# Optimization experiments

Hardware: AMD Instinct MI355X
Metric: run time of the kernel (lower is better)

The kernel has to match this reference:

```python
import jax, jax.numpy as jnp
import numpy as np

EPS = 1e-6
STRIDE = 2  # kv_pool_stride
NUM_HEADS = 8

def _layernorm(x, w, b):
    mu = jnp.mean(x, axis=-1, keepdims=True)
    var = jnp.mean(jnp.square(x - mu), axis=-1, keepdims=True)
    return (x - mu) * jax.lax.rsqrt(var + EPS) * w + b

def setup_inputs() -> dict:
    key = jax.random.key(0)
    B, H, W, C = 8, 56, 56, 384
    hidden = int(C * 2.0)
    ks = jax.random.split(key, 12)
    s = 0.02
    return {
        "x": jax.random.normal(ks[0], (B, H * W, C), jnp.float32),
        "ln1_w": jnp.ones((C,), jnp.float32),
        "ln1_b": jnp.zeros((C,), jnp.float32),
        "qw": jax.random.normal(ks[1], (C, C), jnp.float32) * s,
        "qb": jnp.zeros((C,), jnp.float32),
        "kw": jax.random.normal(ks[2], (C, C), jnp.float32) * s,
        "kb": jnp.zeros((C,), jnp.float32),
        "vw": jax.random.normal(ks[3], (C, C), jnp.float32) * s,
        "vb": jnp.zeros((C,), jnp.float32),
        "pw": jax.random.normal(ks[4], (C, C), jnp.float32) * s,
        "pb": jnp.zeros((C,), jnp.float32),
        "ln2_w": jnp.ones((C,), jnp.float32),
        "ln2_b": jnp.zeros((C,), jnp.float32),
        "fc1_w": jax.random.normal(ks[5], (C, hidden), jnp.float32) * s,
        "fc1_b": jnp.zeros((hidden,), jnp.float32),
        "fc2_w": jax.random.normal(ks[6], (hidden, C), jnp.float32) * s,
        "fc2_b": jnp.zeros((C,), jnp.float32),
        "H": 56,
        "W": 56,
    }

def reference(x, ln1_w, ln1_b, qw, qb, kw, kb, vw, vb, pw, pb,
              ln2_w, ln2_b, fc1_w, fc1_b, fc2_w, fc2_b, H, W):
    B, N, C = x.shape
    h = NUM_HEADS
    d = C // h
    scale = d ** -0.5

    # Attention branch: Q from norm1(x); K,V from RAW x (as in source), KV avg-pooled 2x2
    q_tok = _layernorm(x, ln1_w, ln1_b)
    s = STRIDE
    Hk, Wk = H // s, W // s
    kv = x.reshape(B, Hk, s, Wk, s, C).mean(axis=(2, 4)).reshape(B, Hk * Wk, C)

    q = (q_tok @ qw + qb).reshape(B, N, h, d)
    k = (kv @ kw + kb).reshape(B, Hk * Wk, h, d)
    v = (kv @ vw + vb).reshape(B, Hk * Wk, h, d)

    attn = jnp.einsum('bqhd,bkhd->bhqk', q, k) * scale
    attn = jax.nn.softmax(attn, axis=-1)
    out = jnp.einsum('bhqk,bkhd->bqhd', attn, v).reshape(B, N, C)
    x = x + (out @ pw + pb)

    # MLP branch (GELU exact, matching torch nn.GELU default)
    y = _layernorm(x, ln2_w, ln2_b)
    y = jax.nn.gelu(y @ fc1_w + fc1_b, approximate=False)
    x = x + (y @ fc2_w + fc2_b)
    return x
```

## Files before the change

kernel.cpp:

```cpp
#include <hip/hip_runtime.h>
#include <math.h>

#define B_    8
#define N_TOK 3136
#define C_    384
#define DH    48
#define NK    784
#define HID   768
#define M1    25088
#define M2    6272
#define M1Q   6272

typedef unsigned short u16;
typedef __attribute__((ext_vector_type(8))) short bf16x8;
typedef __attribute__((ext_vector_type(4))) float f32x4;

__device__ __forceinline__ float b2f(u16 u) {
  return __uint_as_float(((unsigned)u) << 16);
}
__device__ __forceinline__ u16 f2b(float f) {
  unsigned u = __float_as_uint(f);
  return (u16)((u + 0x7fffu + ((u >> 16) & 1u)) >> 16);
}
__device__ __forceinline__ u16 f2b_trunc(float f) {
  return (u16)(__float_as_uint(f) >> 16);
}
__device__ __forceinline__ void gload_lds16(const u16* g, u16* l) {
  __builtin_amdgcn_global_load_lds(
      (const __attribute__((address_space(1))) void*)g,
      (__attribute__((address_space(3))) void*)l, 16, 0, 0);
}

__global__ __launch_bounds__(256) void ln1_pool(
    const float* __restrict__ X, const float* __restrict__ w,
    const float* __restrict__ b, u16* __restrict__ Y, u16* __restrict__ KV) {
  if (blockIdx.x < M1 / 4) {
    const int row = blockIdx.x * 4 + (threadIdx.x >> 6);
    const int lane = threadIdx.x & 63;
    const size_t base = (size_t)row * C_;
    float v[6];
#pragma unroll
    for (int i = 0; i < 6; ++i) v[i] = X[base + lane + 64 * i];
    float s = 0.f;
#pragma unroll
    for (int i = 0; i < 6; ++i) s += v[i];
#pragma unroll
    for (int off = 32; off > 0; off >>= 1) s += __shfl_xor(s, off);
    const float mu = s * (1.0f / C_);
    float q = 0.f;
#pragma unroll
    for (int i = 0; i < 6; ++i) { float d = v[i] - mu; q += d * d; }
#pragma unroll
    for (int off = 32; off > 0; off >>= 1) q += __shfl_xor(q, off);
    const float r = rsqrtf(q * (1.0f / C_) + 1e-6f);
#pragma unroll
    for (int i = 0; i < 6; ++i) {
      int c = lane + 64 * i;
      Y[base + c] = f2b((v[i] - mu) * r * w[c] + b[c]);
    }
  } else {
    int t = (blockIdx.x - M1 / 4) * 256 + threadIdx.x;
    if (t >= M2 * C_) return;
    int c = t % C_;
    int row = t / C_;
    int bb = row / NK;
    int rr = row - bb * NK;
    int hk = rr / 28;
    int wk = rr - hk * 28;
    const float* p = X + ((size_t)(bb * N_TOK + hk * 112 + wk * 2)) * C_ + c;
    KV[t] = f2b(0.25f * (p[0] + p[C_] + p[56 * C_] + p[57 * C_]));
  }
}

__global__ __launch_bounds__(256) void ln2_rows(const u16* __restrict__ X,
    const float* __restrict__ w, const float* __restrict__ b, u16* __restrict__ Y) {
  const int row = blockIdx.x * 4 + (threadIdx.x >> 6);
  const int lane = threadIdx.x & 63;
  const size_t base = (size_t)row * C_;
  float v[6];
#pragma unroll
  for (int i = 0; i < 6; ++i) v[i] = b2f(X[base + lane + 64 * i]);
  float s = 0.f;
#pragma unroll
  for (int i = 0; i < 6; ++i) s += v[i];
#pragma unroll
  for (int off = 32; off > 0; off >>= 1) s += __shfl_xor(s, off);
  const float mu = s * (1.0f / C_);
  float q = 0.f;
#pragma unroll
  for (int i = 0; i < 6; ++i) { float d = v[i] - mu; q += d * d; }
#pragma unroll
  for (int off = 32; off > 0; off >>= 1) q += __shfl_xor(q, off);
  const float r = rsqrtf(q * (1.0f / C_) + 1e-6f);
#pragma unroll
  for (int i = 0; i < 6; ++i) {
    int c = lane + 64 * i;
    Y[base + c] = f2b((v[i] - mu) * r * w[c] + b[c]);
  }
}

struct TransArgs {
  const float* src[6];
  u16* dst[6];
  int K[6], N[6], tx[6], ty[6];
};
__global__ __launch_bounds__(256) void transpose_all(TransArgs a) {
  const int id = blockIdx.z;
  if ((int)blockIdx.x >= a.tx[id] || (int)blockIdx.y >= a.ty[id]) return;
  const float* W = a.src[id];
  u16* WT = a.dst[id];
  const int K = a.K[id], N = a.N[id];
  __shared__ u16 tile[64][73];
  const int k0 = blockIdx.y * 64, n0 = blockIdx.x * 64;
  for (int i = threadIdx.x; i < 64 * 64; i += 256) {
    int kk = i >> 6, nn = i & 63;
    tile[kk][nn] = f2b(W[(size_t)(k0 + kk) * N + n0 + nn]);
  }
  __syncthreads();
  for (int i = threadIdx.x; i < 64 * 64; i += 256) {
    int nn = i >> 6, kk = i & 63;
    WT[(size_t)(n0 + nn) * K + k0 + kk] = tile[kk][nn];
  }
}

template<int EPI, bool RES32, bool OUT32>
__device__ __forceinline__ void gemm_core(
    const u16* __restrict__ A, const u16* __restrict__ BT,
    const float* __restrict__ bias, const void* __restrict__ resv,
    void* __restrict__ Cv, int N, int K, int m0, int n0) {
  __shared__ u16 As[128 * 64];
  __shared__ u16 Bs[128 * 64];
  const int tid  = threadIdx.x;
  const int wave = tid >> 6;
  const int lane = tid & 63;
  const int quad = lane >> 4;
  const int ll   = lane & 15;
  const int wm   = wave >> 1, wn = wave & 1;

  const int srow = wave * 32 + (lane >> 3);
  const int sgs  = lane & 7;

  f32x4 acc[4][4];
#pragma unroll
  for (int i = 0; i < 4; ++i)
#pragma unroll
    for (int j = 0; j < 4; ++j) acc[i][j] = (f32x4){0.f, 0.f, 0.f, 0.f};

  for (int kk0 = 0; kk0 < K; kk0 += 64) {
    __syncthreads();
#pragma unroll
    for (int c = 0; c < 4; ++c) {
      const int r = srow + c * 8;
      const int g = sgs ^ (r & 7);
      gload_lds16(A  + (size_t)(m0 + r) * K + kk0 + g * 8,
                  As + (size_t)(wave * 32 + c * 8) * 64);
      gload_lds16(BT + (size_t)(n0 + r) * K + kk0 + g * 8,
                  Bs + (size_t)(wave * 32 + c * 8) * 64);
    }
    __syncthreads();
#pragma unroll
    for (int ks = 0; ks < 2; ++ks) {
      const int gsw = (quad + 4 * ks) ^ (ll & 7);
      bf16x8 af[4], bfr[4];
#pragma unroll
      for (int im = 0; im < 4; ++im)
        af[im] = *(const bf16x8*)&As[(size_t)(wm * 64 + im * 16 + ll) * 64 + gsw * 8];
#pragma unroll
      for (int jn = 0; jn < 4; ++jn)
        bfr[jn] = *(const bf16x8*)&Bs[(size_t)(wn * 64 + jn * 16 + ll) * 64 + gsw * 8];
#pragma unroll
      for (int im = 0; im < 4; ++im)
#pragma unroll
        for (int jn = 0; jn < 4; ++jn)
          acc[im][jn] = __builtin_amdgcn_mfma_f32_16x16x32_bf16(
              af[im], bfr[jn], acc[im][jn], 0, 0, 0);
    }
  }

  float bb[4];
#pragma unroll
  for (int jn = 0; jn < 4; ++jn) bb[jn] = bias[n0 + wn * 64 + jn * 16 + ll];
#pragma unroll
  for (int im = 0; im < 4; ++im) {
    const int row = m0 + wm * 64 + im * 16 + quad * 4;
#pragma unroll
    for (int jn = 0; jn < 4; ++jn) {
      const int col = n0 + wn * 64 + jn * 16 + ll;
#pragma unroll
      for (int r = 0; r < 4; ++r) {
        float o = acc[im][jn][r] + bb[jn];
        if (EPI == 1) {
          o = 0.5f * o * (1.0f + erff(o * 0.70710678118654752f));
        } else if (EPI == 2) {
          size_t ri = (size_t)(row + r) * N + col;
          o += RES32 ? ((const float*)resv)[ri] : b2f(((const u16*)resv)[ri]);
        }
        if (OUT32) ((float*)Cv)[(size_t)(row + r) * N + col] = o;
        else       ((u16*)Cv)[(size_t)(row + r) * N + col] = f2b(o);
      }
    }
  }
}

template<int EPI, bool RES32, bool OUT32>
__global__ __launch_bounds__(256) void gemm_bt(
    const u16* __restrict__ A, const u16* __restrict__ BT,
    const float* __restrict__ bias, const void* __restrict__ resv,
    void* __restrict__ Cv, int N, int K) {
  gemm_core<EPI, RES32, OUT32>(A, BT, bias, resv, Cv, N, K,
                               blockIdx.y << 7, blockIdx.x << 7);
}

struct QKVArgs {
  const u16* A[3];
  const u16* BT[3];
  const float* bias[3];
  u16* C[3];
  int M[3];
};
__global__ __launch_bounds__(256) void gemm_qkv(QKVArgs a) {
  const int z = blockIdx.z;
  const int m0 = blockIdx.y << 7;
  if (m0 >= a.M[z]) return;
  gemm_core<0, false, false>(a.A[z], a.BT[z], a.bias[z], nullptr, a.C[z],
                             C_, C_, m0, blockIdx.x << 7);
}

#define QS_STR 72
__global__ __launch_bounds__(512) void attn_mfma(
    const u16* __restrict__ Q, const u16* __restrict__ Kb,
    const u16* __restrict__ Vb, u16* __restrict__ O) {
  __shared__ u16 Ks[2][64 * 64];
  __shared__ u16 Vt[2][48 * QS_STR];
  __shared__ u16 Ps[128 * QS_STR];
  const int tid  = threadIdx.x;
  const int wave = tid >> 6;
  const int lane = tid & 63;
  const int quad = lane >> 4;
  const int ll   = lane & 15;
  const int qt   = blockIdx.x;
  const int bh   = blockIdx.y;
  const int b    = bh >> 3, h = bh & 7;
  const int q0   = qt * 128;
  const float scale = 0.14433756729740643f;

  bf16x8 af0, af1;
  {
    int qrow = q0 + wave * 16 + ll;
    if (qrow >= N_TOK) qrow = N_TOK - 1;
    const u16* qp = Q + ((size_t)(b * N_TOK) + qrow) * C_ + h * DH;
    af0 = *(const bf16x8*)(qp + quad * 8);
    if (quad < 2) af1 = *(const bf16x8*)(qp + 32 + quad * 8);
    else          af1 = (bf16x8){0, 0, 0, 0, 0, 0, 0, 0};
  }

  const int krow = (wave << 3) + (lane >> 3);
  const int kgrp = (lane & 7) ^ (lane >> 3);
  const size_t kbase_g = (size_t)(b * NK) * C_ + h * DH + kgrp * 8;

  uint4 vreg;

  {
    int kk = krow; if (kk >= NK) kk = NK - 1;
    gload_lds16(Kb + kbase_g + (size_t)kk * C_, &Ks[0][wave << 9]);
    if (wave < 6) {
      int vk = lane; if (vk >= NK) vk = NK - 1;
      vreg = *(const uint4*)(Vb + ((size_t)(b * NK) + vk) * C_ + h * DH + wave * 8);
      const u16* vp = (const u16*)&vreg;
#pragma unroll
      for (int j = 0; j < 8; ++j)
        Vt[0][(wave * 8 + j) * QS_STR + lane] = vp[j];
    }
  }
  __syncthreads();

  f32x4 Ofr[3] = {{0.f,0.f,0.f,0.f},{0.f,0.f,0.f,0.f},{0.f,0.f,0.f,0.f}};
  float lrow[4] = {0.f, 0.f, 0.f, 0.f};

  for (int t = 0; t < 13; ++t) {
    const int cur = t & 1, nxt = cur ^ 1;
    const int kbase = t * 64;

    if (t < 12) {
      const int knext = kbase + 64;
      int kk = knext + krow; if (kk >= NK) kk = NK - 1;
      gload_lds16(Kb + kbase_g + (size_t)kk * C_, &Ks[nxt][wave << 9]);
      if (wave < 6) {
        int vk = knext + lane; if (vk >= NK) vk = NK - 1;
        vreg = *(const uint4*)(Vb + ((size_t)(b * NK) + vk) * C_ + h * DH + wave * 8);
      }
    }

    f32x4 S[4];
#pragma unroll
    for (int nt = 0; nt < 4; ++nt) {
      const int rb = (nt * 16 + ll) * 64;
      bf16x8 b0 = *(const bf16x8*)&Ks[cur][rb + ((quad    ) ^ (ll & 7)) * 8];
      bf16x8 b1 = *(const bf16x8*)&Ks[cur][rb + ((quad + 4) ^ (ll & 7)) * 8];
      f32x4 acc = {0.f, 0.f, 0.f, 0.f};
      acc = __builtin_amdgcn_mfma_f32_16x16x32_bf16(af0, b0, acc, 0, 0, 0);
      acc = __builtin_amdgcn_mfma_f32_16x16x32_bf16(af1, b1, acc, 0, 0, 0);
      if (kbase + nt * 16 + ll >= NK)
        acc = (f32x4){-1e30f, -1e30f, -1e30f, -1e30f};
      S[nt] = acc;
    }

#pragma unroll
    for (int nt = 0; nt < 4; ++nt) {
      const int g = nt * 2 + (ll >> 3);
      const int gp = g ^ quad;
#pragma unroll
      for (int r = 0; r < 4; ++r) {
        float p = __expf(S[nt][r] * scale);
        lrow[r] += p;
        Ps[(wave * 16 + quad * 4 + r) * QS_STR + (gp << 3) + (ll & 7)] = f2b_trunc(p);
      }
    }

#pragma unroll
    for (int dt = 0; dt < 3; ++dt)
#pragma unroll
      for (int ks = 0; ks < 2; ++ks) {
        const int gp = ((ks << 2) + quad) ^ ((ll >> 2) & 3);
        bf16x8 a = *(const bf16x8*)&Ps[(wave * 16 + ll) * QS_STR + (gp << 3)];
        bf16x8 bb = *(const bf16x8*)&Vt[cur][(dt * 16 + ll) * QS_STR + ks * 32 + quad * 8];
        Ofr[dt] = __builtin_amdgcn_mfma_f32_16x16x32_bf16(a, bb, Ofr[dt], 0, 0, 0);
      }

    if (t < 12 && wave < 6) {
      const u16* vp = (const u16*)&vreg;
#pragma unroll
      for (int j = 0; j < 8; ++j)
        Vt[nxt][(wave * 8 + j) * QS_STR + lane] = vp[j];
    }
    __syncthreads();
  }

#pragma unroll
  for (int msk = 1; msk < 16; msk <<= 1)
#pragma unroll
    for (int r = 0; r < 4; ++r)
      lrow[r] += __shfl_xor(lrow[r], msk);
  float inv[4];
#pragma unroll
  for (int r = 0; r < 4; ++r) inv[r] = 1.0f / lrow[r];
#pragma unroll
  for (int dt = 0; dt < 3; ++dt)
#pragma unroll
    for (int r = 0; r < 4; ++r) {
      int qrow = q0 + wave * 16 + quad * 4 + r;
      if (qrow < N_TOK)
        O[((size_t)b * N_TOK + qrow) * C_ + h * DH + dt * 16 + ll] =
            f2b(Ofr[dt][r] * inv[r]);
    }
}

__global__ __launch_bounds__(256) void marker_fill(
    float* __restrict__ out, size_t n, float val) {
  size_t i = (size_t)blockIdx.x * 256 + threadIdx.x;
  const size_t stride = (size_t)gridDim.x * 256;
  for (; i < n; i += stride) out[i] = 0.f;
  if (blockIdx.x == 0 && threadIdx.x == 0) out[0] = val;
}

extern "C" void kernel_launch(void* const* d_in, const int* in_sizes, int n_in,
                              void* d_out, int out_size, void* d_ws, size_t ws_size,
                              hipStream_t stream) {
  const float* x    = (const float*)d_in[0];
  const float* ln1w = (const float*)d_in[1];
  const float* ln1b = (const float*)d_in[2];
  const float* qw   = (const float*)d_in[3];
  const float* qb   = (const float*)d_in[4];
  const float* kw   = (const float*)d_in[5];
  const float* kb   = (const float*)d_in[6];
  const float* vw   = (const float*)d_in[7];
  const float* vb   = (const float*)d_in[8];
  const float* pw   = (const float*)d_in[9];
  const float* pb   = (const float*)d_in[10];
  const float* ln2w = (const float*)d_in[11];
  const float* ln2b = (const float*)d_in[12];
  const float* fc1w = (const float*)d_in[13];
  const float* fc1b = (const float*)d_in[14];
  const float* fc2w = (const float*)d_in[15];
  const float* fc2b = (const float*)d_in[16];

  const size_t BUF = (size_t)M1 * C_;
  float* outf = (float*)d_out;

  {
    static const int exp_sizes[19] = {
      M1 * C_, C_, C_, C_ * C_, C_, C_ * C_, C_, C_ * C_, C_, C_ * C_, C_,
      C_, C_, C_ * HID, HID, HID * C_, C_, 1, 1};
    int bad = -1;
    if (n_in != 19) bad = 99;
    else {
      for (int i = 0; i < 19; ++i)
        if (in_sizes[i] != exp_sizes[i]) { bad = i; break; }
    }
    if (bad >= 0) {
      marker_fill<<<1024, 256, 0, stream>>>(outf, BUF, 10000.0f + (float)bad);
      return;
    }
  }
  const size_t need_min  = 4096 + 3 * BUF * sizeof(u16);
  const size_t need_full = 4096 + (3 * BUF + (size_t)M1 * HID) * sizeof(u16);
  if (ws_size < need_min) {
    marker_fill<<<1024, 256, 0, stream>>>(outf, BUF, 30000.0f + (float)(ws_size >> 20));
    return;
  }
  const bool full_mlp = (ws_size >= need_full);

  u16* T0 = (u16*)((char*)d_ws + 4096);
  u16* T1 = T0 + BUF;
  u16* U  = T1 + BUF;
  u16* P  = U;
  u16* KB = U + (size_t)M2 * C_;
  u16* VB = U + (size_t)2 * M2 * C_;
  u16* HBq = U;
  u16* HBfull = U + BUF;
  u16* WTb = U + BUF - (size_t)(4 * C_ * C_ + 2 * C_ * HID);
  u16* wtq = WTb;
  u16* wtk = wtq + C_ * C_;
  u16* wtv = wtk + C_ * C_;
  u16* wtp = wtv + C_ * C_;
  u16* wtf1 = wtp + C_ * C_;
  u16* wtf2 = wtf1 + (size_t)C_ * HID;

  {
    TransArgs ta;
    ta.src[0] = qw;   ta.dst[0] = wtq;  ta.K[0] = C_;  ta.N[0] = C_;  ta.tx[0] = 6;  ta.ty[0] = 6;
    ta.src[1] = kw;   ta.dst[1] = wtk;  ta.K[1] = C_;  ta.N[1] = C_;  ta.tx[1] = 6;  ta.ty[1] = 6;
    ta.src[2] = vw;   ta.dst[2] = wtv;  ta.K[2] = C_;  ta.N[2] = C_;  ta.tx[2] = 6;  ta.ty[2] = 6;
    ta.src[3] = pw;   ta.dst[3] = wtp;  ta.K[3] = C_;  ta.N[3] = C_;  ta.tx[3] = 6;  ta.ty[3] = 6;
    ta.src[4] = fc1w; ta.dst[4] = wtf1; ta.K[4] = C_;  ta.N[4] = HID; ta.tx[4] = 12; ta.ty[4] = 6;
    ta.src[5] = fc2w; ta.dst[5] = wtf2; ta.K[5] = HID; ta.N[5] = C_;  ta.tx[5] = 6;  ta.ty[5] = 12;
    transpose_all<<<dim3(12, 12, 6), 256, 0, stream>>>(ta);
  }

  ln1_pool<<<M1 / 4 + (M2 * C_) / 256, 256, 0, stream>>>(x, ln1w, ln1b, T0, P);

  {
    QKVArgs qa;
    qa.A[0] = T0; qa.BT[0] = wtq; qa.bias[0] = qb; qa.C[0] = T1; qa.M[0] = M1;
    qa.A[1] = P;  qa.BT[1] = wtk; qa.bias[1] = kb; qa.C[1] = KB; qa.M[1] = M2;
    qa.A[2] = P;  qa.BT[2] = wtv; qa.bias[2] = vb; qa.C[2] = VB; qa.M[2] = M2;
    gemm_qkv<<<dim3(3, 196, 3), 256, 0, stream>>>(qa);
  }

  attn_mfma<<<dim3(25, 64), 512, 0, stream>>>(T1, KB, VB, T0);

  gemm_bt<2, true, false><<<dim3(3, 196), 256, 0, stream>>>(
      T0, wtp, pb, x, T1, C_, C_);

  ln2_rows<<<M1 / 4, 256, 0, stream>>>(T1, ln2w, ln2b, T0);

  if (full_mlp) {
    gemm_bt<1, false, false><<<dim3(6, 196), 256, 0, stream>>>(
        T0, wtf1, fc1b, nullptr, HBfull, HID, C_);
    gemm_bt<2, false, true><<<dim3(3, 196), 256, 0, stream>>>(
        HBfull, wtf2, fc2b, T1, outf, C_, HID);
  } else {
    for (int qtr = 0; qtr < 4; ++qtr) {
      const size_t ro = (size_t)qtr * M1Q;
      gemm_bt<1, false, false><<<dim3(6, 49), 256, 0, stream>>>(
          T0 + ro * C_, wtf1, fc1b, nullptr, HBq, HID, C_);
      gemm_bt<2, false, true><<<dim3(3, 49), 256, 0, stream>>>(
          HBq, wtf2, fc2b, T1 + ro * C_, outf + ro * C_, C_, HID);
    }
  }
}
```

Measured before the change: 343.4 us.

## Process two 16-row query groups per wave in attention to reuse K/V tiles

Doubles the query rows handled per wave in the attention kernel so each staged K/V tile and the V fragments feed two sets of MFMAs, halving the number of blocks. This cuts redundant K/V global loads and LDS staging per query. It costs more registers, fewer blocks for occupancy and load balance, and some wasted work on the padded final query tile.

```diff
diff --git a/kernel.cpp b/kernel.cpp
--- a/kernel.cpp
+++ b/kernel.cpp
@@ -241,17 +241,24 @@
   const int qt   = blockIdx.x;
   const int bh   = blockIdx.y;
   const int b    = bh >> 3, h = bh & 7;
-  const int q0   = qt * 128;
+  const int q0   = qt * 256;
   const float scale = 0.14433756729740643f;
 
-  bf16x8 af0, af1;
+  bf16x8 afA0, afA1, afB0, afB1;
   {
-    int qrow = q0 + wave * 16 + ll;
-    if (qrow >= N_TOK) qrow = N_TOK - 1;
-    const u16* qp = Q + ((size_t)(b * N_TOK) + qrow) * C_ + h * DH;
-    af0 = *(const bf16x8*)(qp + quad * 8);
-    if (quad < 2) af1 = *(const bf16x8*)(qp + 32 + quad * 8);
-    else          af1 = (bf16x8){0, 0, 0, 0, 0, 0, 0, 0};
+    int qA = q0 + wave * 32 + ll;       if (qA >= N_TOK) qA = N_TOK - 1;
+    int qB = q0 + wave * 32 + 16 + ll;  if (qB >= N_TOK) qB = N_TOK - 1;
+    const u16* pa = Q + ((size_t)(b * N_TOK) + qA) * C_ + h * DH;
+    const u16* pb = Q + ((size_t)(b * N_TOK) + qB) * C_ + h * DH;
+    afA0 = *(const bf16x8*)(pa + quad * 8);
+    afB0 = *(const bf16x8*)(pb + quad * 8);
+    if (quad < 2) {
+      afA1 = *(const bf16x8*)(pa + 32 + quad * 8);
+      afB1 = *(const bf16x8*)(pb + 32 + quad * 8);
+    } else {
+      afA1 = (bf16x8){0, 0, 0, 0, 0, 0, 0, 0};
+      afB1 = (bf16x8){0, 0, 0, 0, 0, 0, 0, 0};
+    }
   }
 
   const int krow = (wave << 3) + (lane >> 3);
@@ -274,8 +281,10 @@
   }
   __syncthreads();
 
-  f32x4 Ofr[3] = {{0.f,0.f,0.f,0.f},{0.f,0.f,0.f,0.f},{0.f,0.f,0.f,0.f}};
-  float lrow[4] = {0.f, 0.f, 0.f, 0.f};
+  f32x4 OfA[3] = {{0.f,0.f,0.f,0.f},{0.f,0.f,0.f,0.f},{0.f,0.f,0.f,0.f}};
+  f32x4 OfB[3] = {{0.f,0.f,0.f,0.f},{0.f,0.f,0.f,0.f},{0.f,0.f,0.f,0.f}};
+  float lrA[4] = {0.f, 0.f, 0.f, 0.f};
+  float lrB[4] = {0.f, 0.f, 0.f, 0.f};
 
   for (int t = 0; t < 13; ++t) {
     const int cur = t & 1, nxt = cur ^ 1;
@@ -291,41 +300,81 @@
       }
     }
 
-    f32x4 S[4];
+    f32x4 SA[4], SB[4];
 #pragma unroll
     for (int nt = 0; nt < 4; ++nt) {
       const int rb = (nt * 16 + ll) * 64;
       bf16x8 b0 = *(const bf16x8*)&Ks[cur][rb + ((quad    ) ^ (ll & 7)) * 8];
       bf16x8 b1 = *(const bf16x8*)&Ks[cur][rb + ((quad + 4) ^ (ll & 7)) * 8];
-      f32x4 acc = {0.f, 0.f, 0.f, 0.f};
-      acc = __builtin_amdgcn_mfma_f32_16x16x32_bf16(af0, b0, acc, 0, 0, 0);
-      acc = __builtin_amdgcn_mfma_f32_16x16x32_bf16(af1, b1, acc, 0, 0, 0);
-      if (kbase + nt * 16 + ll >= NK)
-        acc = (f32x4){-1e30f, -1e30f, -1e30f, -1e30f};
-      S[nt] = acc;
-    }
+      f32x4 aA = {0.f, 0.f, 0.f, 0.f};
+      aA = __builtin_amdgcn_mfma_f32_16x16x32_bf16(afA0, b0, aA, 0, 0, 0);
+      aA = __builtin_amdgcn_mfma_f32_16x16x32_bf16(afA1, b1, aA, 0, 0, 0);
+      f32x4 aB = {0.f, 0.f, 0.f, 0.f};
+      aB = __builtin_amdgcn_mfma_f32_16x16x32_bf16(afB0, b0, aB, 0, 0, 0);
+      aB = __builtin_amdgcn_mfma_f32_16x16x32_bf16(afB1, b1, aB, 0, 0, 0);
+      if (kbase + nt * 16 + ll >= NK) {
+        aA = (f32x4){-1e30f, -1e30f, -1e30f, -1e30f};
+        aB = (f32x4){-1e30f, -1e30f, -1e30f, -1e30f};
+      }
+      SA[nt] = aA; SB[nt] = aB;
+    }
+
+    bf16x8 vf[3][2];
+#pragma unroll
+    for (int dt = 0; dt < 3; ++dt)
+#pragma unroll
+      for (int ks = 0; ks < 2; ++ks)
+        vf[dt][ks] = *(const bf16x8*)&Vt[cur][(dt * 16 + ll) * QS_STR + ks * 32 + quad * 8];
 
 #pragma unroll
     for (int nt = 0; nt < 4; ++nt) {
-      const int g = nt * 2 + (ll >> 3);
-      const int gp = g ^ quad;
+      const int gp = (nt * 2 + (ll >> 3)) ^ quad;
 #pragma unroll
       for (int r = 0; r < 4; ++r) {
-        float p = __expf(S[nt][r] * scale);
-        lrow[r] += p;
+        float p = __expf(SA[nt][r] * scale);
+        lrA[r] += p;
         Ps[(wave * 16 + quad * 4 + r) * QS_STR + (gp << 3) + (ll & 7)] = f2b_trunc(p);
       }
     }
-
-#pragma unroll
-    for (int dt = 0; dt < 3; ++dt)
-#pragma unroll
-      for (int ks = 0; ks < 2; ++ks) {
-        const int gp = ((ks << 2) + quad) ^ ((ll >> 2) & 3);
-        bf16x8 a = *(const bf16x8*)&Ps[(wave * 16 + ll) * QS_STR + (gp << 3)];
-        bf16x8 bb = *(const bf16x8*)&Vt[cur][(dt * 16 + ll) * QS_STR + ks * 32 + quad * 8];
-        Ofr[dt] = __builtin_amdgcn_mfma_f32_16x16x32_bf16(a, bb, Ofr[dt], 0, 0, 0);
-      }
+    {
+      bf16x8 pa0, pa1;
+      {
+        const int g0 = ((0 << 2) + quad) ^ ((ll >> 2) & 3);
+        const int g1 = ((1 << 2) + quad) ^ ((ll >> 2) & 3);
+        pa0 = *(const bf16x8*)&Ps[(wave * 16 + ll) * QS_STR + (g0 << 3)];
+        pa1 = *(const bf16x8*)&Ps[(wave * 16 + ll) * QS_STR + (g1 << 3)];
+      }
+#pragma unroll
+      for (int dt = 0; dt < 3; ++dt) {
+        OfA[dt] = __builtin_amdgcn_mfma_f32_16x16x32_bf16(pa0, vf[dt][0], OfA[dt], 0, 0, 0);
+        OfA[dt] = __builtin_amdgcn_mfma_f32_16x16x32_bf16(pa1, vf[dt][1], OfA[dt], 0, 0, 0);
+      }
+    }
+
+#pragma unroll
+    for (int nt = 0; nt < 4; ++nt) {
+      const int gp = (nt * 2 + (ll >> 3)) ^ quad;
+#pragma unroll
+      for (int r = 0; r < 4; ++r) {
+        float p = __expf(SB[nt][r] * scale);
+        lrB[r] += p;
+        Ps[(wave * 16 + quad * 4 + r) * QS_STR + (gp << 3) + (ll & 7)] = f2b_trunc(p);
+      }
+    }
+    {
+      bf16x8 pb0, pb1;
+      {
+        const int g0 = ((0 << 2) + quad) ^ ((ll >> 2) & 3);
+        const int g1 = ((1 << 2) + quad) ^ ((ll >> 2) & 3);
+        pb0 = *(const bf16x8*)&Ps[(wave * 16 + ll) * QS_STR + (g0 << 3)];
+        pb1 = *(const bf16x8*)&Ps[(wave * 16 + ll) * QS_STR + (g1 << 3)];
+      }
+#pragma unroll
+      for (int dt = 0; dt < 3; ++dt) {
+        OfB[dt] = __builtin_amdgcn_mfma_f32_16x16x32_bf16(pb0, vf[dt][0], OfB[dt], 0, 0, 0);
+        OfB[dt] = __builtin_amdgcn_mfma_f32_16x16x32_bf16(pb1, vf[dt][1], OfB[dt], 0, 0, 0);
+      }
+    }
 
     if (t < 12 && wave < 6) {
       const u16* vp = (const u16*)&vreg;
@@ -339,19 +388,25 @@
 #pragma unroll
   for (int msk = 1; msk < 16; msk <<= 1)
 #pragma unroll
-    for (int r = 0; r < 4; ++r)
-      lrow[r] += __shfl_xor(lrow[r], msk);
-  float inv[4];
-#pragma unroll
-  for (int r = 0; r < 4; ++r) inv[r] = 1.0f / lrow[r];
+    for (int r = 0; r < 4; ++r) {
+      lrA[r] += __shfl_xor(lrA[r], msk);
+      lrB[r] += __shfl_xor(lrB[r], msk);
+    }
+  float invA[4], invB[4];
+#pragma unroll
+  for (int r = 0; r < 4; ++r) { invA[r] = 1.0f / lrA[r]; invB[r] = 1.0f / lrB[r]; }
 #pragma unroll
   for (int dt = 0; dt < 3; ++dt)
 #pragma unroll
     for (int r = 0; r < 4; ++r) {
-      int qrow = q0 + wave * 16 + quad * 4 + r;
-      if (qrow < N_TOK)
-        O[((size_t)b * N_TOK + qrow) * C_ + h * DH + dt * 16 + ll] =
-            f2b(Ofr[dt][r] * inv[r]);
+      int qA = q0 + wave * 32 + quad * 4 + r;
+      if (qA < N_TOK)
+        O[((size_t)b * N_TOK + qA) * C_ + h * DH + dt * 16 + ll] =
+            f2b(OfA[dt][r] * invA[r]);
+      int qB = qA + 16;
+      if (qB < N_TOK)
+        O[((size_t)b * N_TOK + qB) * C_ + h * DH + dt * 16 + ll] =
+            f2b(OfB[dt][r] * invB[r]);
     }
 }
 
@@ -447,7 +502,7 @@
     gemm_qkv<<<dim3(3, 196, 3), 256, 0, stream>>>(qa);
   }
 
-  attn_mfma<<<dim3(25, 64), 512, 0, stream>>>(T1, KB, VB, T0);
+  attn_mfma<<<dim3(13, 64), 512, 0, stream>>>(T1, KB, VB, T0);
 
   gemm_bt<2, true, false><<<dim3(3, 196), 256, 0, stream>>>(
       T0, wtp, pb, x, T1, C_, C_);
```

Result: slower. 360.0 us (+4.8%).

## Compute S transposed so P stays in registers, dropping LDS round-trip

Applied to the files above, without the earlier changes.

The QK^T MFMA now runs with K as the A operand and Q as B, so each lane holds scores for consecutive keys of one query. The exponentiated probabilities are packed straight into bf16 registers as the A operand of the PV MFMA, which removes the Ps shared-memory buffer and its stores and loads. V is written to LDS with a permuted column order to match the new key ordering, and the row-sum reduction becomes two shuffles plus a broadcast. This cuts LDS traffic and footprint, but it depends on the permutation matching the MFMA operand layout exactly.

```diff
diff --git a/kernel.cpp b/kernel.cpp
--- a/kernel.cpp
+++ b/kernel.cpp
@@ -232,7 +232,6 @@
     const u16* __restrict__ Vb, u16* __restrict__ O) {
   __shared__ u16 Ks[2][64 * 64];
   __shared__ u16 Vt[2][48 * QS_STR];
-  __shared__ u16 Ps[128 * QS_STR];
   const int tid  = threadIdx.x;
   const int wave = tid >> 6;
   const int lane = tid & 63;
@@ -244,14 +243,14 @@
   const int q0   = qt * 128;
   const float scale = 0.14433756729740643f;
 
-  bf16x8 af0, af1;
+  bf16x8 qf0, qf1;
   {
     int qrow = q0 + wave * 16 + ll;
     if (qrow >= N_TOK) qrow = N_TOK - 1;
     const u16* qp = Q + ((size_t)(b * N_TOK) + qrow) * C_ + h * DH;
-    af0 = *(const bf16x8*)(qp + quad * 8);
-    if (quad < 2) af1 = *(const bf16x8*)(qp + 32 + quad * 8);
-    else          af1 = (bf16x8){0, 0, 0, 0, 0, 0, 0, 0};
+    qf0 = *(const bf16x8*)(qp + quad * 8);
+    if (quad < 2) qf1 = *(const bf16x8*)(qp + 32 + quad * 8);
+    else          qf1 = (bf16x8){0, 0, 0, 0, 0, 0, 0, 0};
   }
 
   const int krow = (wave << 3) + (lane >> 3);
@@ -259,23 +258,26 @@
   const size_t kbase_g = (size_t)(b * NK) * C_ + h * DH + kgrp * 8;
 
   uint4 vreg;
+  const int vkey  = lane;
+  const int vcol  = ((vkey >> 5) << 5) + (((vkey & 15) >> 2) << 3) +
+                    (((vkey >> 4) & 1) << 2) + (vkey & 3);
 
   {
     int kk = krow; if (kk >= NK) kk = NK - 1;
     gload_lds16(Kb + kbase_g + (size_t)kk * C_, &Ks[0][wave << 9]);
     if (wave < 6) {
-      int vk = lane; if (vk >= NK) vk = NK - 1;
+      int vk = vkey; if (vk >= NK) vk = NK - 1;
       vreg = *(const uint4*)(Vb + ((size_t)(b * NK) + vk) * C_ + h * DH + wave * 8);
       const u16* vp = (const u16*)&vreg;
 #pragma unroll
       for (int j = 0; j < 8; ++j)
-        Vt[0][(wave * 8 + j) * QS_STR + lane] = vp[j];
+        Vt[0][(wave * 8 + j) * QS_STR + vcol] = vp[j];
     }
   }
   __syncthreads();
 
   f32x4 Ofr[3] = {{0.f,0.f,0.f,0.f},{0.f,0.f,0.f,0.f},{0.f,0.f,0.f,0.f}};
-  float lrow[4] = {0.f, 0.f, 0.f, 0.f};
+  float lsum = 0.f;
 
   for (int t = 0; t < 13; ++t) {
     const int cur = t & 1, nxt = cur ^ 1;
@@ -286,7 +288,7 @@
       int kk = knext + krow; if (kk >= NK) kk = NK - 1;
       gload_lds16(Kb + kbase_g + (size_t)kk * C_, &Ks[nxt][wave << 9]);
       if (wave < 6) {
-        int vk = knext + lane; if (vk >= NK) vk = NK - 1;
+        int vk = knext + vkey; if (vk >= NK) vk = NK - 1;
         vreg = *(const uint4*)(Vb + ((size_t)(b * NK) + vk) * C_ + h * DH + wave * 8);
       }
     }
@@ -295,55 +297,54 @@
 #pragma unroll
     for (int nt = 0; nt < 4; ++nt) {
       const int rb = (nt * 16 + ll) * 64;
-      bf16x8 b0 = *(const bf16x8*)&Ks[cur][rb + ((quad    ) ^ (ll & 7)) * 8];
-      bf16x8 b1 = *(const bf16x8*)&Ks[cur][rb + ((quad + 4) ^ (ll & 7)) * 8];
+      bf16x8 k0f = *(const bf16x8*)&Ks[cur][rb + ((quad    ) ^ (ll & 7)) * 8];
+      bf16x8 k1f = *(const bf16x8*)&Ks[cur][rb + ((quad + 4) ^ (ll & 7)) * 8];
       f32x4 acc = {0.f, 0.f, 0.f, 0.f};
-      acc = __builtin_amdgcn_mfma_f32_16x16x32_bf16(af0, b0, acc, 0, 0, 0);
-      acc = __builtin_amdgcn_mfma_f32_16x16x32_bf16(af1, b1, acc, 0, 0, 0);
-      if (kbase + nt * 16 + ll >= NK)
-        acc = (f32x4){-1e30f, -1e30f, -1e30f, -1e30f};
+      acc = __builtin_amdgcn_mfma_f32_16x16x32_bf16(k0f, qf0, acc, 0, 0, 0);
+      acc = __builtin_amdgcn_mfma_f32_16x16x32_bf16(k1f, qf1, acc, 0, 0, 0);
       S[nt] = acc;
     }
 
+    unsigned pw[8];
 #pragma unroll
     for (int nt = 0; nt < 4; ++nt) {
-      const int g = nt * 2 + (ll >> 3);
-      const int gp = g ^ quad;
-#pragma unroll
-      for (int r = 0; r < 4; ++r) {
-        float p = __expf(S[nt][r] * scale);
-        lrow[r] += p;
-        Ps[(wave * 16 + quad * 4 + r) * QS_STR + (gp << 3) + (ll & 7)] = f2b_trunc(p);
+#pragma unroll
+      for (int rr = 0; rr < 2; ++rr) {
+        const int key0 = kbase + nt * 16 + quad * 4 + rr * 2;
+        float p0 = (key0     < NK) ? __expf(S[nt][rr * 2    ] * scale) : 0.f;
+        float p1 = (key0 + 1 < NK) ? __expf(S[nt][rr * 2 + 1] * scale) : 0.f;
+        lsum += p0 + p1;
+        pw[nt * 2 + rr] = (__float_as_uint(p0) >> 16) |
+                          (__float_as_uint(p1) & 0xffff0000u);
       }
     }
-
-#pragma unroll
-    for (int dt = 0; dt < 3; ++dt)
-#pragma unroll
-      for (int ks = 0; ks < 2; ++ks) {
-        const int gp = ((ks << 2) + quad) ^ ((ll >> 2) & 3);
-        bf16x8 a = *(const bf16x8*)&Ps[(wave * 16 + ll) * QS_STR + (gp << 3)];
-        bf16x8 bb = *(const bf16x8*)&Vt[cur][(dt * 16 + ll) * QS_STR + ks * 32 + quad * 8];
-        Ofr[dt] = __builtin_amdgcn_mfma_f32_16x16x32_bf16(a, bb, Ofr[dt], 0, 0, 0);
-      }
+    union PU { unsigned w[4]; bf16x8 v; };
+    PU pk0, pk1;
+#pragma unroll
+    for (int i = 0; i < 4; ++i) { pk0.w[i] = pw[i]; pk1.w[i] = pw[4 + i]; }
+
+#pragma unroll
+    for (int dt = 0; dt < 3; ++dt) {
+      bf16x8 v0 = *(const bf16x8*)&Vt[cur][(dt * 16 + ll) * QS_STR + quad * 8];
+      bf16x8 v1 = *(const bf16x8*)&Vt[cur][(dt * 16 + ll) * QS_STR + 32 + quad * 8];
+      Ofr[dt] = __builtin_amdgcn_mfma_f32_16x16x32_bf16(pk0.v, v0, Ofr[dt], 0, 0, 0);
+      Ofr[dt] = __builtin_amdgcn_mfma_f32_16x16x32_bf16(pk1.v, v1, Ofr[dt], 0, 0, 0);
+    }
 
     if (t < 12 && wave < 6) {
       const u16* vp = (const u16*)&vreg;
 #pragma unroll
       for (int j = 0; j < 8; ++j)
-        Vt[nxt][(wave * 8 + j) * QS_STR + lane] = vp[j];
+        Vt[nxt][(wave * 8 + j) * QS_STR + vcol] = vp[j];
     }
     __syncthreads();
   }
 
-#pragma unroll
-  for (int msk = 1; msk < 16; msk <<= 1)
-#pragma unroll
-    for (int r = 0; r < 4; ++r)
-      lrow[r] += __shfl_xor(lrow[r], msk);
+  lsum += __shfl_xor(lsum, 16);
+  lsum += __shfl_xor(lsum, 32);
   float inv[4];
 #pragma unroll
-  for (int r = 0; r < 4; ++r) inv[r] = 1.0f / lrow[r];
+  for (int r = 0; r < 4; ++r) inv[r] = 1.0f / __shfl(lsum, quad * 4 + r);
 #pragma unroll
   for (int dt = 0; dt < 3; ++dt)
 #pragma unroll
```

New measurement: 339.4 us. About the same (-1.2%).
